# Performance work log

Hardware: AMD Instinct MI355X
Metric: run time of the kernel (lower is better)

The kernel has to match this reference:

```python
import jax, jax.numpy as jnp
import numpy as np

DIM = 512
HEAD_DIM = 32
HEADS = DIM // HEAD_DIM
WS = 7              # window_size
DISP = WS // 2      # cyclic shift displacement
SHIFTED = True


def _rel_indices(ws):
    # torch indexes pos_embedding with raw (possibly negative) distances;
    # negative python indices wrap modulo the dim size (2*ws-1).
    idx = np.array([[x, y] for x in range(ws) for y in range(ws)])
    d = idx[None, :, :] - idx[:, None, :]          # (ws^2, ws^2, 2)
    return np.mod(d, 2 * ws - 1)


def _mask(ws, disp, upper_lower, left_right):
    m = np.zeros((ws, ws, ws, ws), np.float32)
    if upper_lower:
        m[:-disp, :, -disp:, :] = -np.inf
        m[-disp:, :, :-disp, :] = -np.inf
    if left_right:
        m[:, -disp:, :, :-disp] = -np.inf
        m[:, :-disp, :, -disp:] = -np.inf
    return m.reshape(ws * ws, ws * ws)


def setup_inputs() -> dict:
    key = jax.random.key(0)
    ks = jax.random.split(key, 5)
    B, H, W = 32, 56, 56
    x = jax.random.normal(ks[0], (B, H, W, DIM), jnp.float32)
    w_qkv = jax.random.normal(ks[1], (DIM, 3 * DIM), jnp.float32) * 0.02
    pos_emb = jax.random.normal(ks[2], (2 * WS - 1, 2 * WS - 1, HEADS), jnp.float32)
    w_out = jax.random.normal(ks[3], (DIM, DIM), jnp.float32) * 0.02
    b_out = jax.random.normal(ks[4], (DIM,), jnp.float32) * 0.02
    return {"x": x, "w_qkv": w_qkv, "pos_emb": pos_emb, "w_out": w_out, "b_out": b_out}


def reference(x, w_qkv, pos_emb, w_out, b_out):
    rel = _rel_indices(WS)                         # static int constants
    ul_mask = jnp.asarray(_mask(WS, DISP, True, False))
    lr_mask = jnp.asarray(_mask(WS, DISP, False, True))

    B, H, W, _ = x.shape
    nw_h, nw_w = H // WS, W // WS

    if SHIFTED:
        x = jnp.roll(x, (-DISP, -DISP), axis=(1, 2))

    qkv = x @ w_qkv                                # (B,H,W,3*dim)

    def to_windows(t):
        # (B,H,W,dim) -> (B, heads, nw_h*nw_w, ws*ws, head_dim)
        t = t.reshape(B, nw_h, WS, nw_w, WS, HEADS, HEAD_DIM)
        return t.transpose(0, 5, 1, 3, 2, 4, 6).reshape(B, HEADS, nw_h * nw_w, WS * WS, HEAD_DIM)

    q, k, v = (to_windows(t) for t in jnp.split(qkv, 3, axis=-1))

    dots = jnp.einsum('bhwid,bhwjd->bhwij', q, k) * (HEAD_DIM ** -0.5)
    bias = pos_emb[rel[:, :, 0], rel[:, :, 1], :]  # (ws^2, ws^2, heads)
    dots = dots + bias.transpose(2, 0, 1)[None, :, None]

    if SHIFTED:
        dots = dots.at[:, :, -nw_w:].add(ul_mask)
        dots = dots.at[:, :, nw_w - 1::nw_w].add(lr_mask)

    attn = jax.nn.softmax(dots, axis=-1)
    out = jnp.einsum('bhwij,bhwjd->bhwid', attn, v)

    # (B,heads,nw,ws^2,d) -> (B,H,W,dim)
    out = out.reshape(B, HEADS, nw_h, nw_w, WS, WS, HEAD_DIM)
    out = out.transpose(0, 2, 4, 3, 5, 1, 6).reshape(B, H, W, DIM)
    out = out @ w_out + b_out

    if SHIFTED:
        out = jnp.roll(out, (DISP, DISP), axis=(1, 2))
    return out
```

## Files before the change

### kernel.cpp

```cpp
#include <hip/hip_runtime.h>
#include <hip/hip_bf16.h>
#include <stdint.h>


#define NWIN 64
#define NTOK 49
#define WIN_ELEMS 1568
#define HEAD_STRIDE 100352
#define BATCH_STRIDE 1605632
#define QKV_ELEMS 51380224
#define NTOKENS 100352
#define SCALE 0.17677669529663687f

typedef __attribute__((ext_vector_type(8))) short bf16x8;
typedef __attribute__((ext_vector_type(4))) float f32x4;

#define AS1 __attribute__((address_space(1)))
#define AS3 __attribute__((address_space(3)))

struct __align__(16) bf8 { __hip_bfloat16 h[8]; };

__device__ __forceinline__ void gload_lds16(const void* g, void* l) {
  __builtin_amdgcn_global_load_lds((const AS1 unsigned int*)g,
                                   (AS3 unsigned int*)l, 16, 0, 0);
}

__device__ __forceinline__ void token_decode(int t, int& b, int& i, int& j) {
  b = t / 3136;
  int r = t - b * 3136;
  i = r / 56;
  j = r - i * 56;
}

__global__ __launch_bounds__(256) void k_prep_lut(int* __restrict__ lutw,
                                                  int* __restrict__ luto) {
  int t = blockIdx.x * 256 + threadIdx.x;
  int b, i, j;
  token_decode(t, b, i, j);
  int win = (i / 7) * 8 + (j / 7);
  int pos = (i % 7) * 7 + (j % 7);
  lutw[t] = b * BATCH_STRIDE + win * WIN_ELEMS + pos * 32;
  int di = i + 3; if (di >= 56) di -= 56;
  int dj = j + 3; if (dj >= 56) dj -= 56;
  luto[t] = ((b * 56 + di) * 56 + dj) * 512;
}

__global__ __launch_bounds__(256) void k_prep_x(const float* __restrict__ x,
                                                __hip_bfloat16* __restrict__ xb) {
  int idx = blockIdx.x * 256 + threadIdx.x;
  int t = idx >> 6;
  int g = idx & 63;
  int b, i, j;
  token_decode(t, b, i, j);
  int si = i + 3; if (si >= 56) si -= 56;
  int sj = j + 3; if (sj >= 56) sj -= 56;
  const float* src = x + ((size_t)(b * 56 + si) * 56 + sj) * 512 + g * 8;
  float4 a0 = *(const float4*)src;
  float4 a1 = *(const float4*)(src + 4);
  bf8 o;
  o.h[0] = __float2bfloat16(a0.x); o.h[1] = __float2bfloat16(a0.y);
  o.h[2] = __float2bfloat16(a0.z); o.h[3] = __float2bfloat16(a0.w);
  o.h[4] = __float2bfloat16(a1.x); o.h[5] = __float2bfloat16(a1.y);
  o.h[6] = __float2bfloat16(a1.z); o.h[7] = __float2bfloat16(a1.w);
  int slot = ((g * 8) ^ ((t & 7) << 3));
  *(bf8*)(xb + (size_t)t * 512 + slot) = o;
}

__global__ __launch_bounds__(256) void k_transpose(const float* __restrict__ in,
                                                   __hip_bfloat16* __restrict__ out,
                                                   int K, int N) {
  __shared__ float tl[64][65];
  const int nb = blockIdx.x * 64, kb = blockIdx.y * 64;
  const int tid = threadIdx.x;
#pragma unroll
  for (int s = 0; s < 16; ++s) {
    int idx = s * 256 + tid; int r = idx >> 6, c = idx & 63;
    tl[r][c] = in[(size_t)(kb + r) * N + nb + c];
  }
  __syncthreads();
#pragma unroll
  for (int s = 0; s < 16; ++s) {
    int idx = s * 256 + tid; int r = idx >> 6, c = idx & 63;
    int row = nb + r;
    int col = (kb + c) ^ ((row & 7) << 3);
    out[(size_t)row * K + col] = __float2bfloat16(tl[c][r]);
  }
}

__global__ __launch_bounds__(256) void k_prep_bias(const float* __restrict__ pe,
                                                   float* __restrict__ biasT) {
  int id = blockIdx.x * 256 + threadIdx.x;
  int whid = id >> 12;
  int wtype = whid >> 4, h = whid & 15;
  int mid = id & 4095;
  int mf = mid >> 10, r = (mid >> 8) & 3, lane = (mid >> 2) & 63, nf = mid & 3;
  int key = mf * 16 + (lane >> 4) * 4 + r;
  int query = nf * 16 + (lane & 15);
  float v;
  if (key >= 49 || query >= 49) {
    v = -1e30f;
  } else {
    int i = query, j = key;
    int xi = i / 7, yi = i - xi * 7;
    int xj = j / 7, yj = j - xj * 7;
    int dx = xj - xi; if (dx < 0) dx += 13;
    int dy = yj - yi; if (dy < 0) dy += 13;
    v = pe[(dx * 13 + dy) * 16 + h];
    if ((wtype & 1) && ((xi >= 4) != (xj >= 4))) v = -1e30f;
    if ((wtype & 2) && ((yi >= 4) != (yj >= 4))) v = -1e30f;
  }
  biasT[id] = v;
}

__global__ __launch_bounds__(256) void k_qkv_mfma(
    const __hip_bfloat16* __restrict__ xb, const __hip_bfloat16* __restrict__ wbt,
    const int* __restrict__ lutw,
    __hip_bfloat16* __restrict__ qb, __hip_bfloat16* __restrict__ kb,
    __hip_bfloat16* __restrict__ vb) {
  __shared__ __align__(16) short As[128 * 64];
  __shared__ __align__(16) short Bs[128 * 64];
  const int tid = threadIdx.x;
  const int lid = blockIdx.x;
  const int wid = (lid & 7) * 1176 + (lid >> 3);
  const int t0 = (wid / 12) * 128;
  const int n0 = (wid % 12) * 128;
  const int lane = tid & 63, wave = tid >> 6;
  const int wm = wave >> 1, wn = wave & 1;

  const __hip_bfloat16* asrc[4];
  const __hip_bfloat16* bsrc[4];
#pragma unroll
  for (int s = 0; s < 4; ++s) {
    int c = s * 256 + tid;
    int row = c >> 3, kc = c & 7;
    asrc[s] = xb + (size_t)(t0 + row) * 512 + kc * 8;
    bsrc[s] = wbt + (size_t)(n0 + row) * 512 + kc * 8;
  }
  char* abase = (char*)As + wave * 1024;
  char* bbase = (char*)Bs + wave * 1024;

  f32x4 acc[4][4] = {};
  const int arow = wm * 64 + (lane & 15);
  const int brow = wn * 64 + (lane & 15);
  const int koff = (lane >> 4) * 8;
  const int sw = (lane & 7) << 3;

  for (int kt = 0; kt < 512; kt += 64) {
#pragma unroll
    for (int s = 0; s < 4; ++s) gload_lds16(asrc[s] + kt, abase + s * 4096);
#pragma unroll
    for (int s = 0; s < 4; ++s) gload_lds16(bsrc[s] + kt, bbase + s * 4096);
    __syncthreads();
    bf16x8 af[2][4], bfr[2][4];
#pragma unroll
    for (int kk = 0; kk < 2; ++kk) {
      const int eo = (kk * 32 + koff) ^ sw;
#pragma unroll
      for (int mf = 0; mf < 4; ++mf)
        af[kk][mf] = *(const bf16x8*)&As[(arow + mf * 16) * 64 + eo];
#pragma unroll
      for (int nf = 0; nf < 4; ++nf)
        bfr[kk][nf] = *(const bf16x8*)&Bs[(brow + nf * 16) * 64 + eo];
    }
#pragma unroll
    for (int kk = 0; kk < 2; ++kk)
#pragma unroll
      for (int mf = 0; mf < 4; ++mf)
#pragma unroll
        for (int nf = 0; nf < 4; ++nf)
          acc[mf][nf] = __builtin_amdgcn_mfma_f32_16x16x32_bf16(
              af[kk][mf], bfr[kk][nf], acc[mf][nf], 0, 0, 0);
    __syncthreads();
  }

  __hip_bfloat16* obs[4];
#pragma unroll
  for (int nf = 0; nf < 4; ++nf) {
    int n = n0 + wn * 64 + nf * 16 + (lane & 15);
    int sp = n >> 9, hc = n & 511, h = hc >> 5, d = hc & 31;
    obs[nf] = (sp == 0 ? qb : (sp == 1 ? kb : vb)) + (size_t)h * HEAD_STRIDE + d;
  }
  const int tbase = t0 + wm * 64 + (lane >> 4) * 4;
  int woff[4][4];
#pragma unroll
  for (int mf = 0; mf < 4; ++mf)
#pragma unroll
    for (int r = 0; r < 4; ++r)
      woff[mf][r] = lutw[tbase + mf * 16 + r];
#pragma unroll
  for (int mf = 0; mf < 4; ++mf)
#pragma unroll
    for (int r = 0; r < 4; ++r) {
      size_t off = (size_t)woff[mf][r];
#pragma unroll
      for (int nf = 0; nf < 4; ++nf)
        obs[nf][off] = __float2bfloat16(acc[mf][nf][r]);
    }
}

__global__ __launch_bounds__(256) void k_attn_mfma(
    const __hip_bfloat16* __restrict__ qb, const __hip_bfloat16* __restrict__ kb,
    const __hip_bfloat16* __restrict__ vb, const float* __restrict__ biasT,
    __hip_bfloat16* __restrict__ ab) {
  __shared__ __align__(16) __hip_bfloat16 P[4][64 * 72];
  __shared__ __align__(16) __hip_bfloat16 VT[4][32 * 64];
  const int tid = threadIdx.x, lane = tid & 63, wave = tid >> 6;
  const int gid = blockIdx.x * 4 + wave;
  const int win = gid & 63, h = (gid >> 6) & 15;
  const int wtype = (((win >> 3) == 7) ? 1 : 0) | (((win & 7) == 7) ? 2 : 0);
  const size_t qkbase = (size_t)gid * WIN_ELEMS;
  const int fr = lane & 15, fo = (lane >> 4) * 8;

  bf8 v8[4];
#pragma unroll
  for (int it = 0; it < 4; ++it) {
    int c = it * 64 + lane;
    if (c < 196) v8[it] = *(const bf8*)(vb + qkbase + (size_t)c * 8);
  }

  bf16x8 kf[4], qf[4];
#pragma unroll
  for (int f = 0; f < 4; ++f) {
    kf[f] = *(const bf16x8*)(kb + qkbase + (size_t)(f * 16 + fr) * 32 + fo);
    qf[f] = *(const bf16x8*)(qb + qkbase + (size_t)(f * 16 + fr) * 32 + fo);
  }

  __hip_bfloat16* vtw = VT[wave];
  {
    bf16x8 zz = {};
#pragma unroll
    for (int z = 0; z < 4; ++z) *(bf16x8*)&vtw[z * 512 + lane * 8] = zz;
  }
#pragma unroll
  for (int it = 0; it < 4; ++it) {
    int c = it * 64 + lane;
    if (c < 196) {
      int pos = c >> 2, d0 = (c & 3) * 8;
#pragma unroll
      for (int u = 0; u < 8; ++u) {
        int d = d0 + u;
        vtw[d * 64 + (pos ^ ((d & 7) << 3))] = v8[it].h[u];
      }
    }
  }

  f32x4 sacc[4][4] = {};
#pragma unroll
  for (int mf = 0; mf < 4; ++mf)
#pragma unroll
    for (int nf = 0; nf < 4; ++nf)
      sacc[mf][nf] = __builtin_amdgcn_mfma_f32_16x16x32_bf16(
          kf[mf], qf[nf], sacc[mf][nf], 0, 0, 0);

  const float* bp = biasT + (size_t)(wtype * 16 + h) * 4096;
#pragma unroll
  for (int mf = 0; mf < 4; ++mf)
#pragma unroll
    for (int r = 0; r < 4; ++r) {
      float4 bv = *(const float4*)(bp + ((mf * 4 + r) * 64 + lane) * 4);
      sacc[mf][0][r] = fmaf(sacc[mf][0][r], SCALE, bv.x);
      sacc[mf][1][r] = fmaf(sacc[mf][1][r], SCALE, bv.y);
      sacc[mf][2][r] = fmaf(sacc[mf][2][r], SCALE, bv.z);
      sacc[mf][3][r] = fmaf(sacc[mf][3][r], SCALE, bv.w);
    }

  float inv[4];
#pragma unroll
  for (int nf = 0; nf < 4; ++nf) {
    float m = sacc[0][nf][0];
#pragma unroll
    for (int mf = 0; mf < 4; ++mf)
#pragma unroll
      for (int r = 0; r < 4; ++r) m = fmaxf(m, sacc[mf][nf][r]);
    m = fmaxf(m, __shfl_xor(m, 16));
    m = fmaxf(m, __shfl_xor(m, 32));
    float sum = 0.f;
#pragma unroll
    for (int mf = 0; mf < 4; ++mf)
#pragma unroll
      for (int r = 0; r < 4; ++r) {
        float e = __expf(sacc[mf][nf][r] - m);
        sacc[mf][nf][r] = e;
        sum += e;
      }
    sum += __shfl_xor(sum, 16);
    sum += __shfl_xor(sum, 32);
    inv[nf] = 1.0f / sum;
  }

  __hip_bfloat16* pw = P[wave];
#pragma unroll
  for (int mf = 0; mf < 4; ++mf)
#pragma unroll
    for (int r = 0; r < 4; ++r) {
      int key = mf * 16 + (lane >> 4) * 4 + r;
#pragma unroll
      for (int nf = 0; nf < 4; ++nf) {
        int query = nf * 16 + fr;
        pw[query * 72 + key] = __float2bfloat16(sacc[mf][nf][r] * inv[nf]);
      }
    }

  f32x4 oacc[4][2] = {};
#pragma unroll
  for (int kk = 0; kk < 2; ++kk) {
    bf16x8 vf[2];
#pragma unroll
    for (int n2 = 0; n2 < 2; ++n2) {
      int d = n2 * 16 + fr;
      vf[n2] = *(const bf16x8*)&vtw[d * 64 + ((kk * 32 + fo) ^ ((d & 7) << 3))];
    }
#pragma unroll
    for (int mf = 0; mf < 4; ++mf) {
      bf16x8 pa = *(const bf16x8*)&pw[(mf * 16 + fr) * 72 + kk * 32 + fo];
#pragma unroll
      for (int n2 = 0; n2 < 2; ++n2)
        oacc[mf][n2] = __builtin_amdgcn_mfma_f32_16x16x32_bf16(
            pa, vf[n2], oacc[mf][n2], 0, 0, 0);
    }
  }

#pragma unroll
  for (int mf = 0; mf < 4; ++mf)
#pragma unroll
    for (int r = 0; r < 4; ++r) {
      int row = mf * 16 + (lane >> 4) * 4 + r;
      if (row < 49) {
#pragma unroll
        for (int n2 = 0; n2 < 2; ++n2)
          ab[qkbase + (size_t)row * 32 + n2 * 16 + fr] =
              __float2bfloat16(oacc[mf][n2][r]);
      }
    }
}

__global__ __launch_bounds__(256) void k_out_mfma(
    const __hip_bfloat16* __restrict__ ab, const __hip_bfloat16* __restrict__ wot,
    const int* __restrict__ lutw, const int* __restrict__ luto,
    const float* __restrict__ bias, float* __restrict__ out) {
  __shared__ __align__(16) short As[128 * 64];
  __shared__ __align__(16) short Bs[128 * 64];
  const int tid = threadIdx.x;
  const int lid = blockIdx.x;
  const int wid = (lid & 7) * 392 + (lid >> 3);
  const int t0 = (wid >> 2) * 128;
  const int n0 = (wid & 3) * 128;
  const int lane = tid & 63, wave = tid >> 6;
  const int wm = wave >> 1, wn = wave & 1;

  size_t aoff[4];
  const __hip_bfloat16* bsrc[4];
#pragma unroll
  for (int s = 0; s < 4; ++s) {
    int c = s * 256 + tid;
    int row = c >> 3, kc = c & 7;
    aoff[s] = (size_t)lutw[t0 + row] + (size_t)(kc >> 2) * HEAD_STRIDE + (kc & 3) * 8;
    bsrc[s] = wot + (size_t)(n0 + row) * 512 + kc * 8;
  }

  f32x4 acc[4][4] = {};
  const int arow = wm * 64 + (lane & 15);
  const int brow = wn * 64 + (lane & 15);
  const int koff = (lane >> 4) * 8;
  const int sw = (lane & 7) << 3;

  for (int kt = 0; kt < 512; kt += 64) {
    size_t hoff = (size_t)(kt >> 5) * HEAD_STRIDE;
#pragma unroll
    for (int s = 0; s < 4; ++s) {
      gload_lds16(ab + aoff[s] + hoff, (char*)As + wave * 1024 + s * 4096);
      gload_lds16(bsrc[s] + kt, (char*)Bs + wave * 1024 + s * 4096);
    }
    __syncthreads();
    bf16x8 af[2][4], bfr[2][4];
#pragma unroll
    for (int kk = 0; kk < 2; ++kk) {
      const int eo = kk * 32 + koff;
#pragma unroll
      for (int mf = 0; mf < 4; ++mf)
        af[kk][mf] = *(const bf16x8*)&As[(arow + mf * 16) * 64 + eo];
#pragma unroll
      for (int nf = 0; nf < 4; ++nf)
        bfr[kk][nf] = *(const bf16x8*)&Bs[(brow + nf * 16) * 64 + (eo ^ sw)];
    }
#pragma unroll
    for (int kk = 0; kk < 2; ++kk)
#pragma unroll
      for (int mf = 0; mf < 4; ++mf)
#pragma unroll
        for (int nf = 0; nf < 4; ++nf)
          acc[mf][nf] = __builtin_amdgcn_mfma_f32_16x16x32_bf16(
              af[kk][mf], bfr[kk][nf], acc[mf][nf], 0, 0, 0);
    __syncthreads();
  }

  float bia[4];
#pragma unroll
  for (int nf = 0; nf < 4; ++nf)
    bia[nf] = bias[n0 + wn * 64 + nf * 16 + (lane & 15)];

  const int tbase = t0 + wm * 64 + (lane >> 4) * 4;
  int ooff[4][4];
#pragma unroll
  for (int mf = 0; mf < 4; ++mf)
#pragma unroll
    for (int r = 0; r < 4; ++r)
      ooff[mf][r] = luto[tbase + mf * 16 + r];
#pragma unroll
  for (int mf = 0; mf < 4; ++mf) {
#pragma unroll
    for (int r = 0; r < 4; ++r) {
      float* op = out + (size_t)ooff[mf][r] + n0 + wn * 64 + (lane & 15);
#pragma unroll
      for (int nf = 0; nf < 4; ++nf) op[nf * 16] = acc[mf][nf][r] + bia[nf];
    }
  }
}

extern "C" void kernel_launch(void* const* d_in, const int* in_sizes, int n_in,
                              void* d_out, int out_size, void* d_ws, size_t ws_size,
                              hipStream_t stream) {
  const float* x     = (const float*)d_in[0];
  const float* w_qkv = (const float*)d_in[1];
  const float* pe    = (const float*)d_in[2];
  const float* w_out = (const float*)d_in[3];
  const float* b_out = (const float*)d_in[4];
  float* out = (float*)d_out;

  __hip_bfloat16* qb  = (__hip_bfloat16*)d_ws;
  __hip_bfloat16* kb  = qb + (size_t)QKV_ELEMS;
  __hip_bfloat16* vb  = kb + (size_t)QKV_ELEMS;
  __hip_bfloat16* xb  = vb + (size_t)QKV_ELEMS;
  __hip_bfloat16* ab  = xb;
  __hip_bfloat16* wbt = xb + (size_t)QKV_ELEMS;
  __hip_bfloat16* wot = wbt + (size_t)(1536 * 512);
  float* biasT = (float*)(wot + (size_t)(512 * 512));
  int* lutw = (int*)(biasT + 262144);
  int* luto = lutw + NTOKENS;

  k_prep_lut<<<dim3(392), dim3(256), 0, stream>>>(lutw, luto);
  k_prep_x<<<dim3(25088), dim3(256), 0, stream>>>(x, xb);
  k_transpose<<<dim3(24, 8), dim3(256), 0, stream>>>(w_qkv, wbt, 512, 1536);
  k_transpose<<<dim3(8, 8), dim3(256), 0, stream>>>(w_out, wot, 512, 512);
  k_prep_bias<<<dim3(1024), dim3(256), 0, stream>>>(pe, biasT);
  k_qkv_mfma<<<dim3(9408), dim3(256), 0, stream>>>(xb, wbt, lutw, qb, kb, vb);
  k_attn_mfma<<<dim3(8192), dim3(256), 0, stream>>>(qb, kb, vb, biasT, ab);
  k_out_mfma<<<dim3(3136), dim3(256), 0, stream>>>(ab, wot, lutw, luto, b_out, out);
}
```

Measured before the change: 561.5 us.

## Double-buffer LDS tiles in QKV and output projection GEMMs

```diff
diff --git a/kernel.cpp b/kernel.cpp
--- a/kernel.cpp
+++ b/kernel.cpp
@@ -117,8 +117,8 @@
     const int* __restrict__ lutw,
     __hip_bfloat16* __restrict__ qb, __hip_bfloat16* __restrict__ kb,
     __hip_bfloat16* __restrict__ vb) {
-  __shared__ __align__(16) short As[128 * 64];
-  __shared__ __align__(16) short Bs[128 * 64];
+  __shared__ __align__(16) short As[2][128 * 64];
+  __shared__ __align__(16) short Bs[2][128 * 64];
   const int tid = threadIdx.x;
   const int lid = blockIdx.x;
   const int wid = (lid & 7) * 1176 + (lid >> 3);
@@ -136,8 +136,6 @@
     asrc[s] = xb + (size_t)(t0 + row) * 512 + kc * 8;
     bsrc[s] = wbt + (size_t)(n0 + row) * 512 + kc * 8;
   }
-  char* abase = (char*)As + wave * 1024;
-  char* bbase = (char*)Bs + wave * 1024;
 
   f32x4 acc[4][4] = {};
   const int arow = wm * 64 + (lane & 15);
@@ -145,23 +143,40 @@
   const int koff = (lane >> 4) * 8;
   const int sw = (lane & 7) << 3;
 
-  for (int kt = 0; kt < 512; kt += 64) {
-#pragma unroll
-    for (int s = 0; s < 4; ++s) gload_lds16(asrc[s] + kt, abase + s * 4096);
-#pragma unroll
-    for (int s = 0; s < 4; ++s) gload_lds16(bsrc[s] + kt, bbase + s * 4096);
-    __syncthreads();
+#pragma unroll
+  for (int s = 0; s < 4; ++s) {
+    gload_lds16(asrc[s], (char*)As[0] + wave * 1024 + s * 4096);
+    gload_lds16(bsrc[s], (char*)Bs[0] + wave * 1024 + s * 4096);
+  }
+
+  for (int t = 0; t < 8; ++t) {
+    const int buf = t & 1;
+    if (t < 7) {
+      const int kt = (t + 1) * 64;
+#pragma unroll
+      for (int s = 0; s < 4; ++s) {
+        gload_lds16(asrc[s] + kt, (char*)As[buf ^ 1] + wave * 1024 + s * 4096);
+        gload_lds16(bsrc[s] + kt, (char*)Bs[buf ^ 1] + wave * 1024 + s * 4096);
+      }
+      asm volatile("s_waitcnt vmcnt(8)" ::: "memory");
+    } else {
+      asm volatile("s_waitcnt vmcnt(0)" ::: "memory");
+    }
+    __builtin_amdgcn_s_barrier();
+    __builtin_amdgcn_sched_barrier(0);
+
     bf16x8 af[2][4], bfr[2][4];
 #pragma unroll
     for (int kk = 0; kk < 2; ++kk) {
       const int eo = (kk * 32 + koff) ^ sw;
 #pragma unroll
       for (int mf = 0; mf < 4; ++mf)
-        af[kk][mf] = *(const bf16x8*)&As[(arow + mf * 16) * 64 + eo];
+        af[kk][mf] = *(const bf16x8*)&As[buf][(arow + mf * 16) * 64 + eo];
 #pragma unroll
       for (int nf = 0; nf < 4; ++nf)
-        bfr[kk][nf] = *(const bf16x8*)&Bs[(brow + nf * 16) * 64 + eo];
-    }
+        bfr[kk][nf] = *(const bf16x8*)&Bs[buf][(brow + nf * 16) * 64 + eo];
+    }
+    __builtin_amdgcn_s_setprio(1);
 #pragma unroll
     for (int kk = 0; kk < 2; ++kk)
 #pragma unroll
@@ -170,7 +185,9 @@
         for (int nf = 0; nf < 4; ++nf)
           acc[mf][nf] = __builtin_amdgcn_mfma_f32_16x16x32_bf16(
               af[kk][mf], bfr[kk][nf], acc[mf][nf], 0, 0, 0);
-    __syncthreads();
+    __builtin_amdgcn_s_setprio(0);
+    __builtin_amdgcn_s_barrier();
+    __builtin_amdgcn_sched_barrier(0);
   }
 
   __hip_bfloat16* obs[4];
@@ -338,8 +355,8 @@
     const __hip_bfloat16* __restrict__ ab, const __hip_bfloat16* __restrict__ wot,
     const int* __restrict__ lutw, const int* __restrict__ luto,
     const float* __restrict__ bias, float* __restrict__ out) {
-  __shared__ __align__(16) short As[128 * 64];
-  __shared__ __align__(16) short Bs[128 * 64];
+  __shared__ __align__(16) short As[2][128 * 64];
+  __shared__ __align__(16) short Bs[2][128 * 64];
   const int tid = threadIdx.x;
   const int lid = blockIdx.x;
   const int wid = (lid & 7) * 392 + (lid >> 3);
@@ -364,25 +381,41 @@
   const int koff = (lane >> 4) * 8;
   const int sw = (lane & 7) << 3;
 
-  for (int kt = 0; kt < 512; kt += 64) {
-    size_t hoff = (size_t)(kt >> 5) * HEAD_STRIDE;
-#pragma unroll
-    for (int s = 0; s < 4; ++s) {
-      gload_lds16(ab + aoff[s] + hoff, (char*)As + wave * 1024 + s * 4096);
-      gload_lds16(bsrc[s] + kt, (char*)Bs + wave * 1024 + s * 4096);
-    }
-    __syncthreads();
+#pragma unroll
+  for (int s = 0; s < 4; ++s) {
+    gload_lds16(ab + aoff[s], (char*)As[0] + wave * 1024 + s * 4096);
+    gload_lds16(bsrc[s], (char*)Bs[0] + wave * 1024 + s * 4096);
+  }
+
+  for (int t = 0; t < 8; ++t) {
+    const int buf = t & 1;
+    if (t < 7) {
+      const int kt = (t + 1) * 64;
+      size_t hoff = (size_t)(kt >> 5) * HEAD_STRIDE;
+#pragma unroll
+      for (int s = 0; s < 4; ++s) {
+        gload_lds16(ab + aoff[s] + hoff, (char*)As[buf ^ 1] + wave * 1024 + s * 4096);
+        gload_lds16(bsrc[s] + kt, (char*)Bs[buf ^ 1] + wave * 1024 + s * 4096);
+      }
+      asm volatile("s_waitcnt vmcnt(8)" ::: "memory");
+    } else {
+      asm volatile("s_waitcnt vmcnt(0)" ::: "memory");
+    }
+    __builtin_amdgcn_s_barrier();
+    __builtin_amdgcn_sched_barrier(0);
+
     bf16x8 af[2][4], bfr[2][4];
 #pragma unroll
     for (int kk = 0; kk < 2; ++kk) {
       const int eo = kk * 32 + koff;
 #pragma unroll
       for (int mf = 0; mf < 4; ++mf)
-        af[kk][mf] = *(const bf16x8*)&As[(arow + mf * 16) * 64 + eo];
+        af[kk][mf] = *(const bf16x8*)&As[buf][(arow + mf * 16) * 64 + eo];
 #pragma unroll
       for (int nf = 0; nf < 4; ++nf)
-        bfr[kk][nf] = *(const bf16x8*)&Bs[(brow + nf * 16) * 64 + (eo ^ sw)];
-    }
+        bfr[kk][nf] = *(const bf16x8*)&Bs[buf][(brow + nf * 16) * 64 + (eo ^ sw)];
+    }
+    __builtin_amdgcn_s_setprio(1);
 #pragma unroll
     for (int kk = 0; kk < 2; ++kk)
 #pragma unroll
@@ -391,7 +424,9 @@
         for (int nf = 0; nf < 4; ++nf)
           acc[mf][nf] = __builtin_amdgcn_mfma_f32_16x16x32_bf16(
               af[kk][mf], bfr[kk][nf], acc[mf][nf], 0, 0, 0);
-    __syncthreads();
+    __builtin_amdgcn_s_setprio(0);
+    __builtin_amdgcn_s_barrier();
+    __builtin_amdgcn_sched_barrier(0);
   }
 
   float bia[4];
```

Result: faster. 542.4 us (-3.4%).
